# Performance work log

Hardware: AMD Instinct MI355X
Metric: run time of the kernel (lower is better)

The kernel has to match this reference:

```python
import jax, jax.numpy as jnp
import numpy as np

B, M, R = 32768, 64, 16

def setup_inputs() -> dict:
    key = jax.random.key(0)
    # x: [B, M, R, 2] real/imag stacked, matching the torch module's input layout
    x = jax.random.normal(key, (B, M, R, 2), dtype=jnp.float32)
    return {"x": x}

def reference(x) -> jnp.ndarray:
    # Combine real/imag channels into a complex matrix per batch element.
    xc = jax.lax.complex(x[..., 0], x[..., 1])  # [B, M, R] complex64
    # Batched reduced QR (replaces the Python loop of per-batch torch.linalg.qr).
    q, _ = jnp.linalg.qr(xc, mode="reduced")    # q: [B, M, R] complex64
    # Split back into stacked real/imag channels: [B, M, R, 2]
    return jnp.stack([q.real, q.imag], axis=-1)
```

## Files before the change

### kernel.cpp

```cpp
#include <hip/hip_runtime.h>


constexpr int Mrows = 64;
constexpr int Rcols = 16;

typedef int v2i __attribute__((ext_vector_type(2)));
typedef float v2f __attribute__((ext_vector_type(2)));

#if defined(__has_builtin)
#if __has_builtin(__builtin_amdgcn_permlane16_swap)
#define USE_PL16 1
#else
#define USE_PL16 0
#endif
#if __has_builtin(__builtin_amdgcn_permlane32_swap)
#define USE_PL32 1
#else
#define USE_PL32 0
#endif
#else
#define USE_PL16 0
#define USE_PL32 0
#endif

__device__ __forceinline__ float rdlane(float v, int srclane) {
  return __int_as_float(__builtin_amdgcn_readlane(__float_as_int(v), srclane));
}

__device__ __forceinline__ float plswap16_addf(float v) {
#if USE_PL16
  v2i r = __builtin_amdgcn_permlane16_swap(__float_as_int(v), __float_as_int(v),
                                           false, false);
  return __int_as_float(r[0]) + __int_as_float(r[1]);
#else
  return v + __shfl_xor(v, 16, 64);
#endif
}

__device__ __forceinline__ float plswap32_addf(float v) {
#if USE_PL32
  v2i r = __builtin_amdgcn_permlane32_swap(__float_as_int(v), __float_as_int(v),
                                           false, false);
  return __int_as_float(r[0]) + __int_as_float(r[1]);
#else
  return v + __shfl_xor(v, 32, 64);
#endif
}

__device__ __forceinline__ v2f pkfma(v2f a, v2f b, v2f c) {
#if defined(__has_builtin) && __has_builtin(__builtin_elementwise_fma)
  return __builtin_elementwise_fma(a, b, c);
#else
  v2f r;
  r[0] = fmaf(a[0], b[0], c[0]);
  r[1] = fmaf(a[1], b[1], c[1]);
  return r;
#endif
}

__device__ __forceinline__ v2f splat2(float s) { v2f r; r[0] = s; r[1] = s; return r; }

template <int IMM>
__device__ __forceinline__ float dswz(float v) {
  return __int_as_float(__builtin_amdgcn_ds_swizzle(__float_as_int(v), IMM));
}

template <int I>
__device__ __forceinline__ void get_u(int h, bool g0, float dr, float di,
                                      const v2f (&Ar2)[8], const v2f (&Ai2)[8],
                                      v2f& t, v2f& s) {
  constexpr int IH = I / 2;
  constexpr int ILo = I % 2;
  constexpr int SWZ = (I << 5) | 0x10;
  t[0] = dswz<SWZ>(Ar2[h][0]);
  t[1] = dswz<SWZ>(Ar2[h][1]);
  s[0] = dswz<SWZ>(Ai2[h][0]);
  s[1] = dswz<SWZ>(Ai2[h][1]);
  const v2f z2 = splat2(0.f);
  if (I > 0 && h < IH) {
    t = g0 ? z2 : t;
    s = g0 ? z2 : s;
  }
  if (h == IH) {
    if (ILo == 1) {
      t[0] = g0 ? 0.f : t[0];
      s[0] = g0 ? 0.f : s[0];
      t[1] = g0 ? dr : t[1];
      s[1] = g0 ? di : s[1];
    } else {
      t[0] = g0 ? dr : t[0];
      s[0] = g0 ? di : s[0];
    }
  }
}

template <int CTRL, int RM>
__device__ __forceinline__ double dpp_dadd(double v) {
  union { double d; int i[2]; } u, s;
  u.d = v;
  s.i[0] = __builtin_amdgcn_update_dpp(0, u.i[0], CTRL, RM, 0xF, true);
  s.i[1] = __builtin_amdgcn_update_dpp(0, u.i[1], CTRL, RM, 0xF, true);
  return v + s.d;
}

__device__ __forceinline__ double rdlaned(double v, int srclane) {
  union { double d; int i[2]; } u, r;
  u.d = v;
  r.i[0] = __builtin_amdgcn_readlane(u.i[0], srclane);
  r.i[1] = __builtin_amdgcn_readlane(u.i[1], srclane);
  return r.d;
}

__device__ __forceinline__ double wsum64d_fast(double v) {
  v = dpp_dadd<0xB1, 0xF>(v);
  v = dpp_dadd<0x4E, 0xF>(v);
  v = dpp_dadd<0x141, 0xF>(v);
  v = dpp_dadd<0x140, 0xF>(v);
  v = dpp_dadd<0x142, 0xA>(v);
  v = dpp_dadd<0x143, 0xC>(v);
  return rdlaned(v, 63);
}

__device__ void qr_f64_fused(const float* __restrict__ x,
                             float* __restrict__ out, int b, int lane) {
  const float4* xp = reinterpret_cast<const float4*>(
      x + (size_t)b * (Mrows * Rcols * 2) + (size_t)lane * (Rcols * 2));
  double xr[Rcols], xi[Rcols], ar[Rcols], ai[Rcols];
#pragma unroll
  for (int k = 0; k < Rcols / 2; ++k) {
    float4 t = xp[k];
    xr[2 * k] = (double)t.x;      xi[2 * k] = (double)t.y;
    xr[2 * k + 1] = (double)t.z;  xi[2 * k + 1] = (double)t.w;
  }
#pragma unroll
  for (int j = 0; j < Rcols; ++j) { ar[j] = xr[j]; ai[j] = xi[j]; }

#pragma unroll
  for (int i = 0; i < Rcols; ++i) {
    double cr = ar[i], ci = ai[i];
    double sq = (lane > i) ? (cr * cr + ci * ci) : 0.0;
    double xnorm2 = wsum64d_fast(sq);
    double alphr = rdlaned(cr, i);
    double alphi = rdlaned(ci, i);

    double tr, ti;
    if (xnorm2 == 0.0 && alphi == 0.0) {
      tr = 0.0;  ti = 0.0;
    } else {
      double nrm = sqrt(alphr * alphr + alphi * alphi + xnorm2);
      double beta = (alphr >= 0.0) ? -nrm : nrm;
      double rb = 1.0 / beta;
      tr = (beta - alphr) * rb;
      ti = -alphi * rb;
      double dr = alphr - beta, di = alphi;
      double inv = 1.0 / (dr * dr + di * di);
      double sr = dr * inv, si = -di * inv;
      if (lane > i) {
        double nr = cr * sr - ci * si;
        double ni = cr * si + ci * sr;
        ar[i] = nr;
        ai[i] = ni;
      }
      if (lane == i) { ar[i] = beta; ai[i] = 0.0; }
    }

    double vr = (lane == i) ? 1.0 : ((lane > i) ? ar[i] : 0.0);
    double vi = (lane == i) ? 0.0 : ((lane > i) ? ai[i] : 0.0);
    const double ctr = tr, cti = -ti;
#pragma unroll
    for (int j = i + 1; j < Rcols; ++j) {
      double pr = fma(vr, ar[j], vi * ai[j]);
      double pi = fma(vr, ai[j], -(vi * ar[j]));
      pr = wsum64d_fast(pr);
      pi = wsum64d_fast(pi);
      double wr = fma(ctr, pr, -(cti * pi));
      double wi = fma(ctr, pi, cti * pr);
      ar[j] = fma(-wr, vr, fma(wi, vi, ar[j]));
      ai[j] = fma(-wr, vi, fma(-wi, vr, ai[j]));
    }

    double swr = xr[i], swi = xi[i];
#pragma unroll
    for (int k = 0; k < Rcols; ++k) {
      if (k >= i) break;
      double rr = rdlaned(ar[i], k);
      double ri = rdlaned(ai[i], k);
      swr = fma(-xr[k], rr, fma(xi[k], ri, swr));
      swi = fma(-xr[k], ri, fma(-xi[k], rr, swi));
    }
    double rbd = 1.0 / rdlaned(ar[i], i);
    xr[i] = swr * rbd;
    xi[i] = swi * rbd;
  }

  float4* op = reinterpret_cast<float4*>(
      out + (size_t)b * (Mrows * Rcols * 2) + (size_t)lane * (Rcols * 2));
#pragma unroll
  for (int k = 0; k < Rcols / 2; ++k) {
    op[k] = make_float4((float)xr[2 * k], (float)xi[2 * k],
                        (float)xr[2 * k + 1], (float)xi[2 * k + 1]);
  }
}

template <int I>
__device__ __forceinline__ void qr_step(int lane,
                                        v2f (&Ar2)[8], v2f (&Ai2)[8],
                                        v2f (&Pr2)[8], v2f (&Pi2)[8],
                                        float& S, int bpaR, bool& risky) {
  const int c = lane & 15;
  const bool g0 = (lane < 16);
  constexpr int IH = I / 2;
  constexpr int ILo = I % 2;
  constexpr int SWZ = (I << 5) | 0x10;
  const v2f z2 = splat2(0.f);

  float alphr = rdlane(Ar2[IH][ILo], I);
  float alphi = rdlane(Ai2[IH][ILo], I);
  float SI = rdlane(S, I);
  float xnorm2 = fmaxf(SI - fmaf(alphr, alphr, alphi * alphi), 0.f);
  risky = risky || (fabsf(alphr) < 2e-4f);

  float ctr, cti, dr, di, beta_s;
  if (xnorm2 == 0.f && alphi == 0.f) {
    ctr = 0.f; cti = 0.f; dr = 0.f; di = 0.f;
    beta_s = alphr;
  } else {
    float nrm = __builtin_amdgcn_sqrtf(
        fmaf(alphr, alphr, fmaf(alphi, alphi, xnorm2)));
    float beta = (alphr >= 0.f) ? -nrm : nrm;
    float rbeta = __builtin_amdgcn_rcpf(beta);
    float tr = (beta - alphr) * rbeta;
    float ti = -alphi * rbeta;
    dr = alphr - beta;  di = alphi;
    float inv = __builtin_amdgcn_rcpf(fmaf(dr, dr, di * di));
    ctr = tr * inv;
    cti = -(ti * inv);
    beta_s = beta;
  }
  float rbq = __builtin_amdgcn_rcpf(beta_s);

  v2f prv = z2, piv = z2;
#pragma unroll
  for (int h = 0; h < 8; ++h) {
    v2f t, s;
    get_u<I>(h, g0, dr, di, Ar2, Ai2, t, s);
    prv = pkfma(t, Ar2[h], pkfma(s, Ai2[h], prv));
    piv = pkfma(t, Ai2[h], pkfma(-s, Ar2[h], piv));
  }
  float pr = prv[0] + prv[1];
  float pi = piv[0] + piv[1];
  pr = plswap16_addf(pr);  pr = plswap32_addf(pr);
  pi = plswap16_addf(pi);  pi = plswap32_addf(pi);
  const bool cle = (c <= I);
  pr = cle ? 0.f : pr;
  pi = cle ? 0.f : pi;

  float wr = fmaf(ctr, pr, -(cti * pi));
  float wi = fmaf(ctr, pi, cti * pr);
  const v2f wrv = splat2(wr), wiv = splat2(wi);
#pragma unroll
  for (int h = 0; h < 8; ++h) {
    v2f t, s;
    get_u<I>(h, g0, dr, di, Ar2, Ai2, t, s);
    Ar2[h] = pkfma(-wrv, t, pkfma(wiv, s, Ar2[h]));
    Ai2[h] = pkfma(-wrv, s, pkfma(-wiv, t, Ai2[h]));
  }

  float rr = __int_as_float(
      __builtin_amdgcn_ds_bpermute(bpaR, __float_as_int(Ar2[IH][ILo])));
  float ri = __int_as_float(
      __builtin_amdgcn_ds_bpermute(bpaR, __float_as_int(Ai2[IH][ILo])));
  const bool ceq = (c == I);
  const bool clt = (c < I);
  rr = ceq ? (beta_s - 1.f) : rr;
  rr = clt ? 0.f : rr;
  ri = cle ? 0.f : ri;

  S = S - fmaf(rr, rr, ri * ri);

  const v2f rrv = splat2(rr * rbq), riv = splat2(ri * rbq);

#pragma unroll
  for (int h = 0; h < 8; ++h) {
    v2f br, bi;
    br[0] = dswz<SWZ>(Pr2[h][0]);
    br[1] = dswz<SWZ>(Pr2[h][1]);
    bi[0] = dswz<SWZ>(Pi2[h][0]);
    bi[1] = dswz<SWZ>(Pi2[h][1]);
    Pr2[h] = pkfma(-br, rrv, pkfma(bi, riv, Pr2[h]));
    Pi2[h] = pkfma(-br, riv, pkfma(-bi, rrv, Pi2[h]));
  }
}

__global__ __launch_bounds__(256)
__attribute__((amdgpu_waves_per_eu(3)))
void qr_fused(const float* __restrict__ x, float* __restrict__ out, int B) {
  const int lane = threadIdx.x & 63;
  const int wave = threadIdx.x >> 6;
  const int b = blockIdx.x * 4 + wave;
  if (b >= B) return;
  const int c = lane & 15;
  const int gbase = lane & 48;
  const int bpaR = c << 2;

  const float2* xp = reinterpret_cast<const float2*>(x) +
                     (size_t)b * (Mrows * Rcols) + (size_t)gbase * Rcols + c;
  v2f Ar2[8], Ai2[8], Pr2[8], Pi2[8];
#pragma unroll
  for (int h = 0; h < 8; ++h) {
    float2 t0 = xp[(2 * h) * Rcols];
    float2 t1 = xp[(2 * h + 1) * Rcols];
    v2f r, s;
    r[0] = t0.x;  r[1] = t1.x;
    s[0] = t0.y;  s[1] = t1.y;
    Ar2[h] = r;  Ai2[h] = s;
    Pr2[h] = r;  Pi2[h] = s;
  }

  v2f s2 = splat2(0.f);
#pragma unroll
  for (int h = 0; h < 8; ++h) {
    s2 = pkfma(Ar2[h], Ar2[h], pkfma(Ai2[h], Ai2[h], s2));
  }
  float S = s2[0] + s2[1];
  S = plswap16_addf(S);
  S = plswap32_addf(S);

  bool risky = false;
  qr_step<0>(lane, Ar2, Ai2, Pr2, Pi2, S, bpaR, risky);
  qr_step<1>(lane, Ar2, Ai2, Pr2, Pi2, S, bpaR, risky);
  qr_step<2>(lane, Ar2, Ai2, Pr2, Pi2, S, bpaR, risky);
  qr_step<3>(lane, Ar2, Ai2, Pr2, Pi2, S, bpaR, risky);
  qr_step<4>(lane, Ar2, Ai2, Pr2, Pi2, S, bpaR, risky);
  qr_step<5>(lane, Ar2, Ai2, Pr2, Pi2, S, bpaR, risky);
  qr_step<6>(lane, Ar2, Ai2, Pr2, Pi2, S, bpaR, risky);
  qr_step<7>(lane, Ar2, Ai2, Pr2, Pi2, S, bpaR, risky);
  qr_step<8>(lane, Ar2, Ai2, Pr2, Pi2, S, bpaR, risky);
  qr_step<9>(lane, Ar2, Ai2, Pr2, Pi2, S, bpaR, risky);
  qr_step<10>(lane, Ar2, Ai2, Pr2, Pi2, S, bpaR, risky);
  qr_step<11>(lane, Ar2, Ai2, Pr2, Pi2, S, bpaR, risky);
  qr_step<12>(lane, Ar2, Ai2, Pr2, Pi2, S, bpaR, risky);
  qr_step<13>(lane, Ar2, Ai2, Pr2, Pi2, S, bpaR, risky);
  qr_step<14>(lane, Ar2, Ai2, Pr2, Pi2, S, bpaR, risky);
  qr_step<15>(lane, Ar2, Ai2, Pr2, Pi2, S, bpaR, risky);

  if (risky) {
    qr_f64_fused(x, out, b, lane);
    return;
  }

  float2* op = reinterpret_cast<float2*>(out) +
               (size_t)b * (Mrows * Rcols) + (size_t)gbase * Rcols + c;
#pragma unroll
  for (int h = 0; h < 8; ++h) {
    op[(2 * h) * Rcols] = make_float2(Pr2[h][0], Pi2[h][0]);
    op[(2 * h + 1) * Rcols] = make_float2(Pr2[h][1], Pi2[h][1]);
  }
}

extern "C" void kernel_launch(void* const* d_in, const int* in_sizes, int n_in,
                              void* d_out, int out_size, void* d_ws,
                              size_t ws_size, hipStream_t stream) {
  const float* x = (const float*)d_in[0];
  float* out = (float*)d_out;
  const int B = in_sizes[0] / (Mrows * Rcols * 2);
  dim3 block(256);
  dim3 grid((B + 3) / 4);
  qr_fused<<<grid, block, 0, stream>>>(x, out, B);
}
```

Baseline: 537.7 us.

## Defer risky batches to a separate f64 fallback kernel via atomic worklist

Instead of running the double-precision fallback inline inside the fast fp32 kernel, which inflates its register footprint and causes divergence, risky batch indices are appended to a workspace list with an atomic counter. A second kernel then processes only the listed batches in f64 using a grid-stride loop. This adds a memset and an extra launch, and when no workspace is provided it falls back to running f64 on every batch, which would be much slower.

Result: slower. 554.0 us, median of 2 (+3.0%).

```diff
diff --git a/kernel.cpp b/kernel.cpp
--- a/kernel.cpp
+++ b/kernel.cpp
@@ -121,8 +121,8 @@
   return rdlaned(v, 63);
 }
 
-__device__ void qr_f64_fused(const float* __restrict__ x,
-                             float* __restrict__ out, int b, int lane) {
+__device__ void qr_f64_one(const float* __restrict__ x,
+                           float* __restrict__ out, int b, int lane) {
   const float4* xp = reinterpret_cast<const float4*>(
       x + (size_t)b * (Mrows * Rcols * 2) + (size_t)lane * (Rcols * 2));
   double xr[Rcols], xi[Rcols], ar[Rcols], ai[Rcols];
@@ -294,7 +294,8 @@
 
 __global__ __launch_bounds__(256)
 __attribute__((amdgpu_waves_per_eu(3)))
-void qr_fused(const float* __restrict__ x, float* __restrict__ out, int B) {
+void qr_fused(const float* __restrict__ x, float* __restrict__ out,
+              int* __restrict__ cnt, int* __restrict__ list, int B) {
   const int lane = threadIdx.x & 63;
   const int wave = threadIdx.x >> 6;
   const int b = blockIdx.x * 4 + wave;
@@ -345,7 +346,10 @@
   qr_step<15>(lane, Ar2, Ai2, Pr2, Pi2, S, bpaR, risky);
 
   if (risky) {
-    qr_f64_fused(x, out, b, lane);
+    if (lane == 0) {
+      int idx = atomicAdd(cnt, 1);
+      list[idx] = b;
+    }
     return;
   }
 
@@ -356,6 +360,25 @@
     op[(2 * h) * Rcols] = make_float2(Pr2[h][0], Pi2[h][0]);
     op[(2 * h + 1) * Rcols] = make_float2(Pr2[h][1], Pi2[h][1]);
   }
+}
+
+__global__ __launch_bounds__(256) void qr_f64_list(
+    const float* __restrict__ x, float* __restrict__ out,
+    const int* __restrict__ cnt, const int* __restrict__ list) {
+  const int lane = threadIdx.x & 63;
+  const int widx = blockIdx.x * 4 + (threadIdx.x >> 6);
+  const int n = *cnt;
+  for (int w = widx; w < n; w += 2048) {
+    qr_f64_one(x, out, list[w], lane);
+  }
+}
+
+__global__ __launch_bounds__(256) void qr_f64_all(
+    const float* __restrict__ x, float* __restrict__ out, int B) {
+  const int lane = threadIdx.x & 63;
+  const int b = blockIdx.x * 4 + (threadIdx.x >> 6);
+  if (b >= B) return;
+  qr_f64_one(x, out, b, lane);
 }
 
 extern "C" void kernel_launch(void* const* d_in, const int* in_sizes, int n_in,
@@ -366,5 +389,15 @@
   const int B = in_sizes[0] / (Mrows * Rcols * 2);
   dim3 block(256);
   dim3 grid((B + 3) / 4);
-  qr_fused<<<grid, block, 0, stream>>>(x, out, B);
-}
+
+  const size_t need_list = 16 + (size_t)B * sizeof(int);
+  if (d_ws && ws_size >= need_list) {
+    int* cnt = (int*)d_ws;
+    int* list = (int*)d_ws + 4;
+    hipMemsetAsync(d_ws, 0, 16, stream);
+    qr_fused<<<grid, block, 0, stream>>>(x, out, cnt, list, B);
+    qr_f64_list<<<dim3(512), block, 0, stream>>>(x, out, cnt, list);
+  } else {
+    qr_f64_all<<<grid, block, 0, stream>>>(x, out, B);
+  }
+}
```
